# Optimization experiments

Measured on AMD Instinct MI355X. Metric: run time of the kernel, lower is better.

Reference implementation:

```python
import jax, jax.numpy as jnp
import numpy as np

B, S, D = 4, 4096, 1024

def setup_inputs() -> dict:
    key = jax.random.key(0)
    kx, kq, kk, kv = jax.random.split(key, 4)
    x = jax.random.normal(kx, (B, S, D), dtype=jnp.float32)
    # nn.Linear weights, stored here as [d_in, d_out] so y = x @ W
    scale = 1.0 / np.sqrt(D)
    Wq = jax.random.normal(kq, (D, D), dtype=jnp.float32) * scale
    Wk = jax.random.normal(kk, (D, D), dtype=jnp.float32) * scale
    Wv = jax.random.normal(kv, (D, D), dtype=jnp.float32) * scale
    return {"x": x, "Wq": Wq, "Wk": Wk, "Wv": Wv}

def reference(x, Wq, Wk, Wv):
    b, n, d_in = x.shape
    d_out = Wk.shape[1]
    q = jnp.einsum('bnd,de->bne', x, Wq)
    k = jnp.einsum('bnd,de,->bne', x, Wk, 1.0)  # keys
    v = jnp.einsum('bnd,de->bne', x, Wv)
    # full causal attention: scores scaled by 1/sqrt(d_out) AFTER masking (matches source)
    scores = jnp.einsum('bqe,bke->bqk', q, k)
    causal = jnp.triu(jnp.ones((n, n), dtype=bool), k=1)  # True above diagonal -> masked
    scores = jnp.where(causal[None, :, :], -jnp.inf, scores)
    attn = jax.nn.softmax(scores / jnp.sqrt(jnp.asarray(d_out, scores.dtype)), axis=-1)
    # dropout p=0.0 (eval) -> identity
    return jnp.einsum('bqk,bke->bqe', attn, v)
```

## Files before the change

### kernel.cpp

```cpp
#include <hip/hip_runtime.h>
#include <hip/hip_bf16.h>

#define B_ 4
#define S_ 4096
#define D_ 1024
#define NT_ 32
#define PAIRS_ 528

typedef __attribute__((ext_vector_type(8))) short short8;
typedef __attribute__((ext_vector_type(4))) float f32x4;

__device__ __forceinline__ unsigned short f2bf(float f) {
    union { float f; unsigned u; } v; v.f = f;
    unsigned u = v.u;
    return (unsigned short)((u + 0x7fffu + ((u >> 16) & 1u)) >> 16);
}

__device__ __forceinline__ void gld_lds16(const unsigned short* g, unsigned short* l) {
    __builtin_amdgcn_global_load_lds((const __attribute__((address_space(1))) void*)g,
                                     (__attribute__((address_space(3))) void*)l, 16, 0, 0);
}

__device__ __forceinline__ void stage128x32(const unsigned short* gbase, size_t ld,
                                            unsigned short* ls, int tid) {
    const int r = tid >> 2;
    const int c = (tid & 3) * 8;
    unsigned short* lw = ls + tid * 8;
    gld_lds16(gbase + (size_t)r * ld + c, lw);
    gld_lds16(gbase + (size_t)(r + 64) * ld + c, lw + 2048);
}

__global__ __launch_bounds__(256) void prep_x(const float* __restrict__ x,
                                              unsigned short* __restrict__ xb) {
    size_t i = ((size_t)blockIdx.x * 256 + threadIdx.x) * 8;
    float4 a = *(const float4*)&x[i];
    float4 b = *(const float4*)&x[i + 4];
    unsigned u0 = (unsigned)f2bf(a.x) | ((unsigned)f2bf(a.y) << 16);
    unsigned u1 = (unsigned)f2bf(a.z) | ((unsigned)f2bf(a.w) << 16);
    unsigned u2 = (unsigned)f2bf(b.x) | ((unsigned)f2bf(b.y) << 16);
    unsigned u3 = (unsigned)f2bf(b.z) | ((unsigned)f2bf(b.w) << 16);
    uint4 val; val.x = u0; val.y = u1; val.z = u2; val.w = u3;
    *(uint4*)&xb[i] = val;
}

__global__ __launch_bounds__(256) void prep_w(const float* __restrict__ Wq,
                                              const float* __restrict__ Wk,
                                              const float* __restrict__ Wv,
                                              unsigned short* __restrict__ Wt) {
    __shared__ float ls[64 * 65];
    const int z = blockIdx.z;
    const float* __restrict__ W = (z == 0) ? Wq : (z == 1) ? Wk : Wv;
    unsigned short* __restrict__ Wtz = Wt + (size_t)z * D_ * D_;
    const int k0 = blockIdx.y * 64, n0 = blockIdx.x * 64;
    const int tid = threadIdx.x;
    #pragma unroll
    for (int i = 0; i < 16; ++i) {
        int lin = i * 256 + tid, r = lin >> 6, c = lin & 63;
        ls[r * 65 + c] = W[(size_t)(k0 + r) * D_ + n0 + c];
    }
    __syncthreads();
    #pragma unroll
    for (int i = 0; i < 16; ++i) {
        int lin = i * 256 + tid, r = lin >> 6, c = lin & 63;
        Wtz[(size_t)(n0 + r) * D_ + k0 + c] = f2bf(ls[c * 65 + r]);
    }
}

__global__ __launch_bounds__(256) void qkv_gemm(
    const unsigned short* __restrict__ xb, const unsigned short* __restrict__ Wt,
    unsigned short* __restrict__ Q, unsigned short* __restrict__ K,
    unsigned short* __restrict__ V)
{
    __shared__ __align__(16) unsigned short lsA[4096];
    __shared__ __align__(16) unsigned short lsB[4096];

    const int z = blockIdx.z;
    unsigned short* __restrict__ Y = (z == 0) ? Q : (z == 1) ? K : V;
    const float scale = (z == 0) ? 0.03125f : 1.0f;

    const int m0 = blockIdx.y * 128, n0 = blockIdx.x * 128;
    const int tid = threadIdx.x, lane = tid & 63, w = tid >> 6;
    const int wm = w >> 1, wn = w & 1, quad = lane >> 4, ln = lane & 15;

    const unsigned short* Ab = xb + (size_t)m0 * D_;
    const unsigned short* Bb = Wt + (size_t)z * D_ * D_ + (size_t)n0 * D_;

    f32x4 acc[4][4] = {};

    for (int et = 0; et < D_ / 32; ++et) {
        stage128x32(Ab + et * 32, D_, lsA, tid);
        stage128x32(Bb + et * 32, D_, lsB, tid);
        __syncthreads();
        short8 af[4], bfr[4];
        #pragma unroll
        for (int mf = 0; mf < 4; ++mf)
            af[mf] = *(const short8*)&lsA[(wm * 64 + mf * 16 + ln) * 32 + quad * 8];
        #pragma unroll
        for (int nf = 0; nf < 4; ++nf)
            bfr[nf] = *(const short8*)&lsB[(wn * 64 + nf * 16 + ln) * 32 + quad * 8];
        #pragma unroll
        for (int mf = 0; mf < 4; ++mf)
            #pragma unroll
            for (int nf = 0; nf < 4; ++nf)
                acc[mf][nf] = __builtin_amdgcn_mfma_f32_16x16x32_bf16(af[mf], bfr[nf], acc[mf][nf], 0, 0, 0);
        __syncthreads();
    }

    #pragma unroll
    for (int mf = 0; mf < 4; ++mf)
        #pragma unroll
        for (int nf = 0; nf < 4; ++nf)
            #pragma unroll
            for (int r = 0; r < 4; ++r) {
                int row = m0 + wm * 64 + mf * 16 + quad * 4 + r;
                int col = n0 + wn * 64 + nf * 16 + ln;
                Y[(size_t)row * D_ + col] = f2bf(acc[mf][nf][r] * scale);
            }
}

__global__ __launch_bounds__(256) void vt_trans(const unsigned short* __restrict__ V,
                                                unsigned short* __restrict__ Vt) {
    __shared__ unsigned short ls[64 * 66];
    const int s0 = blockIdx.x * 64, e0 = blockIdx.y * 64, b = blockIdx.z;
    const int tid = threadIdx.x;
    const size_t base = (size_t)b * S_ * D_;
    #pragma unroll
    for (int i = 0; i < 16; ++i) {
        int lin = i * 256 + tid, r = lin >> 6, c = lin & 63;
        ls[r * 66 + c] = V[base + (size_t)(s0 + r) * D_ + e0 + c];
    }
    __syncthreads();
    const size_t baseT = (size_t)b * D_ * S_;
    #pragma unroll
    for (int i = 0; i < 16; ++i) {
        int lin = i * 256 + tid, r = lin >> 6, c = lin & 63;
        Vt[baseT + (size_t)(e0 + r) * S_ + s0 + c] = ls[c * 66 + r];
    }
}

__global__ __launch_bounds__(256) void qk_pexp(
    const unsigned short* __restrict__ Q, const unsigned short* __restrict__ K,
    unsigned short* __restrict__ P, float* __restrict__ lpart)
{
    __shared__ __align__(16) unsigned short lsA[4096];
    __shared__ __align__(16) unsigned short lsB[4096];
    __shared__ float sml[2][128];

    const int p = blockIdx.x, b = blockIdx.y;
    int qt = (int)((sqrtf(8.0f * (float)p + 1.0f) - 1.0f) * 0.5f);
    while ((qt + 1) * (qt + 2) / 2 <= p) ++qt;
    while (qt * (qt + 1) / 2 > p) --qt;
    const int kt = p - qt * (qt + 1) / 2;

    const int q0 = qt * 128, k0 = kt * 128;
    const int tid = threadIdx.x, lane = tid & 63, w = tid >> 6;
    const int wm = w >> 1, wn = w & 1, quad = lane >> 4, ln = lane & 15;
    const size_t base = (size_t)b * S_ * D_;

    const unsigned short* Qb = Q + base + (size_t)q0 * D_;
    const unsigned short* Kb = K + base + (size_t)k0 * D_;

    f32x4 acc[4][4] = {};
    for (int et = 0; et < D_ / 32; ++et) {
        stage128x32(Qb + et * 32, D_, lsA, tid);
        stage128x32(Kb + et * 32, D_, lsB, tid);
        __syncthreads();
        short8 af[4], bfr[4];
        #pragma unroll
        for (int mf = 0; mf < 4; ++mf)
            af[mf] = *(const short8*)&lsA[(wm * 64 + mf * 16 + ln) * 32 + quad * 8];
        #pragma unroll
        for (int nf = 0; nf < 4; ++nf)
            bfr[nf] = *(const short8*)&lsB[(wn * 64 + nf * 16 + ln) * 32 + quad * 8];
        #pragma unroll
        for (int mf = 0; mf < 4; ++mf)
            #pragma unroll
            for (int nf = 0; nf < 4; ++nf)
                acc[mf][nf] = __builtin_amdgcn_mfma_f32_16x16x32_bf16(af[mf], bfr[nf], acc[mf][nf], 0, 0, 0);
        __syncthreads();
    }

    const bool diag = (kt == qt);
    unsigned short* Pt = P + ((size_t)b * PAIRS_ + p) * (128 * 128);

    #pragma unroll
    for (int mf = 0; mf < 4; ++mf)
        #pragma unroll
        for (int r = 0; r < 4; ++r) {
            int rowq = wm * 64 + mf * 16 + quad * 4 + r;
            float lsum = 0.0f;
            #pragma unroll
            for (int nf = 0; nf < 4; ++nf) {
                int ckey = wn * 64 + nf * 16 + ln;
                float s = acc[mf][nf][r];
                float pe = (diag && ckey > rowq) ? 0.0f : __expf(fminf(s, 60.0f));
                Pt[rowq * 128 + ckey] = f2bf(pe);
                lsum += pe;
            }
            #pragma unroll
            for (int off = 1; off < 16; off <<= 1)
                lsum += __shfl_xor(lsum, off);
            if (ln == 0) sml[wn][rowq] = lsum;
        }
    __syncthreads();

    if (tid < 128)
        lpart[((size_t)b * PAIRS_ + p) * 128 + tid] = sml[0][tid] + sml[1][tid];
}

__global__ __launch_bounds__(128) void merge_il(const float* __restrict__ lpart,
                                                float* __restrict__ il) {
    const int qt = blockIdx.x, b = blockIdx.y;
    const int row = threadIdx.x;
    const int pbase = qt * (qt + 1) / 2;
    float l = 0.0f;
    for (int kt = 0; kt <= qt; ++kt)
        l += lpart[((size_t)b * PAIRS_ + pbase + kt) * 128 + row];
    il[(size_t)b * S_ + qt * 128 + row] = 1.0f / l;
}

__global__ __launch_bounds__(256) void pv_gemm(
    const unsigned short* __restrict__ P, const unsigned short* __restrict__ Vt,
    const float* __restrict__ il, float* __restrict__ O)
{
    __shared__ __align__(16) unsigned short lsA[4096];
    __shared__ __align__(16) unsigned short lsB[4096];

    const int dt = blockIdx.x, b = blockIdx.z;
    const int qt = NT_ - 1 - blockIdx.y;
    const int q0 = qt * 128, d0 = dt * 128;
    const int tid = threadIdx.x, lane = tid & 63, w = tid >> 6;
    const int wm = w >> 1, wn = w & 1, quad = lane >> 4, ln = lane & 15;
    const int pbase = qt * (qt + 1) / 2;

    const unsigned short* Vtb = Vt + ((size_t)b * D_ + d0) * S_;

    f32x4 acc[4][4] = {};

    for (int ktile = 0; ktile <= qt; ++ktile) {
        const unsigned short* Ptile = P + ((size_t)b * PAIRS_ + pbase + ktile) * (128 * 128);
        #pragma unroll 1
        for (int sub = 0; sub < 4; ++sub) {
            stage128x32(Ptile + sub * 32, 128, lsA, tid);
            stage128x32(Vtb + ktile * 128 + sub * 32, S_, lsB, tid);
            __syncthreads();
            short8 af[4], bfr[4];
            #pragma unroll
            for (int mf = 0; mf < 4; ++mf)
                af[mf] = *(const short8*)&lsA[(wm * 64 + mf * 16 + ln) * 32 + quad * 8];
            #pragma unroll
            for (int nf = 0; nf < 4; ++nf)
                bfr[nf] = *(const short8*)&lsB[(wn * 64 + nf * 16 + ln) * 32 + quad * 8];
            #pragma unroll
            for (int mf = 0; mf < 4; ++mf)
                #pragma unroll
                for (int nf = 0; nf < 4; ++nf)
                    acc[mf][nf] = __builtin_amdgcn_mfma_f32_16x16x32_bf16(af[mf], bfr[nf], acc[mf][nf], 0, 0, 0);
            __syncthreads();
        }
    }

    #pragma unroll
    for (int mf = 0; mf < 4; ++mf) {
        float ilv[4];
        #pragma unroll
        for (int r = 0; r < 4; ++r)
            ilv[r] = il[(size_t)b * S_ + q0 + wm * 64 + mf * 16 + quad * 4 + r];
        #pragma unroll
        for (int nf = 0; nf < 4; ++nf)
            #pragma unroll
            for (int r = 0; r < 4; ++r) {
                int rowq = q0 + wm * 64 + mf * 16 + quad * 4 + r;
                int col = d0 + wn * 64 + nf * 16 + ln;
                O[((size_t)b * S_ + rowq) * D_ + col] = acc[mf][nf][r] * ilv[r];
            }
    }
}

extern "C" void kernel_launch(void* const* d_in, const int* in_sizes, int n_in,
                              void* d_out, int out_size, void* d_ws, size_t ws_size,
                              hipStream_t stream) {
    const float* x  = (const float*)d_in[0];
    const float* Wq = (const float*)d_in[1];
    const float* Wk = (const float*)d_in[2];
    const float* Wv = (const float*)d_in[3];

    const size_t nQ = (size_t)B_ * S_ * D_;
    const size_t nP = (size_t)B_ * PAIRS_ * 128 * 128;

    unsigned short* P  = (unsigned short*)d_ws;
    unsigned short* V  = P;
    unsigned short* Q  = P + nP;
    unsigned short* K  = Q + nQ;
    unsigned short* Vt = K + nQ;
    unsigned short* xb = Vt;
    unsigned short* Wt = Vt + nQ;
    float* lpart = (float*)(Wt + (size_t)3 * D_ * D_);
    float* il    = lpart + (size_t)B_ * PAIRS_ * 128;
    float* O = (float*)d_out;

    hipLaunchKernelGGL(prep_x, dim3(8192), dim3(256), 0, stream, x, xb);
    hipLaunchKernelGGL(prep_w, dim3(16, 16, 3), dim3(256), 0, stream, Wq, Wk, Wv, Wt);
    hipLaunchKernelGGL(qkv_gemm, dim3(8, 128, 3), dim3(256), 0, stream, xb, Wt, Q, K, V);
    hipLaunchKernelGGL(vt_trans, dim3(64, 16, B_), dim3(256), 0, stream, V, Vt);
    hipLaunchKernelGGL(qk_pexp, dim3(PAIRS_, B_), dim3(256), 0, stream, Q, K, P, lpart);
    hipLaunchKernelGGL(merge_il, dim3(NT_, B_), dim3(128), 0, stream, lpart, il);
    hipLaunchKernelGGL(pv_gemm, dim3(8, NT_, B_), dim3(256), 0, stream, P, Vt, il, O);
}
```

Before: 496.3 us.

## Remap block indices for XCD locality and widen PV tiles to 128x256

Remaps block indices in qkv_gemm and qk_pexp so that blocks landing on the same XCD share operand tiles and the triangular (qt,kt) work is balanced across XCDs. pv_gemm now computes 128x256 output tiles with 32 accumulators per thread. Each staged P tile is reused across twice as many columns, and the grid shrinks to 512 blocks with a load-balanced qt assignment. This halves P re-reads from global memory, at the cost of more registers and LDS and possibly lower occupancy.

```diff
diff --git a/kernel.cpp b/kernel.cpp
--- a/kernel.cpp
+++ b/kernel.cpp
@@ -78,7 +78,12 @@
     unsigned short* __restrict__ Y = (z == 0) ? Q : (z == 1) ? K : V;
     const float scale = (z == 0) ? 0.03125f : 1.0f;
 
-    const int m0 = blockIdx.y * 128, n0 = blockIdx.x * 128;
+    const int lin = blockIdx.x + 8 * blockIdx.y;
+    const int xcd = lin & 7;
+    const int s = lin >> 3;
+    const int m0 = (xcd * 16 + (s >> 3)) * 128;
+    const int n0 = (s & 7) * 128;
+
     const int tid = threadIdx.x, lane = tid & 63, w = tid >> 6;
     const int wm = w >> 1, wn = w & 1, quad = lane >> 4, ln = lane & 15;
 
@@ -146,11 +151,15 @@
     __shared__ __align__(16) unsigned short lsB[4096];
     __shared__ float sml[2][128];
 
-    const int p = blockIdx.x, b = blockIdx.y;
-    int qt = (int)((sqrtf(8.0f * (float)p + 1.0f) - 1.0f) * 0.5f);
-    while ((qt + 1) * (qt + 2) / 2 <= p) ++qt;
-    while (qt * (qt + 1) / 2 > p) --qt;
-    const int kt = p - qt * (qt + 1) / 2;
+    const int l = blockIdx.x, b = blockIdx.y;
+    const int r = l & 7;
+    const int s = l >> 3;
+    int qt, kt;
+    if (s < r + 1)            { qt = r;      kt = s; }
+    else if (s < 33)          { qt = 31 - r; kt = s - (r + 1); }
+    else if (s < 42 + r)      { qt = 8 + r;  kt = s - 33; }
+    else                      { qt = 23 - r; kt = s - (42 + r); }
+    const int p = qt * (qt + 1) / 2 + kt;
 
     const int q0 = qt * 128, k0 = kt * 128;
     const int tid = threadIdx.x, lane = tid & 63, w = tid >> 6;
@@ -186,14 +195,14 @@
     #pragma unroll
     for (int mf = 0; mf < 4; ++mf)
         #pragma unroll
-        for (int r = 0; r < 4; ++r) {
-            int rowq = wm * 64 + mf * 16 + quad * 4 + r;
+        for (int rr = 0; rr < 4; ++rr) {
+            int rowq = wm * 64 + mf * 16 + quad * 4 + rr;
             float lsum = 0.0f;
             #pragma unroll
             for (int nf = 0; nf < 4; ++nf) {
                 int ckey = wn * 64 + nf * 16 + ln;
-                float s = acc[mf][nf][r];
-                float pe = (diag && ckey > rowq) ? 0.0f : __expf(fminf(s, 60.0f));
+                float sc = acc[mf][nf][rr];
+                float pe = (diag && ckey > rowq) ? 0.0f : __expf(fminf(sc, 60.0f));
                 Pt[rowq * 128 + ckey] = f2bf(pe);
                 lsum += pe;
             }
@@ -224,18 +233,25 @@
     const float* __restrict__ il, float* __restrict__ O)
 {
     __shared__ __align__(16) unsigned short lsA[4096];
-    __shared__ __align__(16) unsigned short lsB[4096];
-
-    const int dt = blockIdx.x, b = blockIdx.z;
-    const int qt = NT_ - 1 - blockIdx.y;
-    const int q0 = qt * 128, d0 = dt * 128;
+    __shared__ __align__(16) unsigned short lsB[8192];
+
+    const int l = blockIdx.x;
+    const int b = l >> 7;
+    const int l7 = l & 127;
+    const int r = l7 & 7;
+    const int s = l7 >> 3;
+    const int g = r >> 2;
+    const int dt = r & 3;
+    const int qt = (g == 0) ? ((s < 8) ? 31 - s : 15 - s) : (23 - s);
+
+    const int q0 = qt * 128, d0 = dt * 256;
     const int tid = threadIdx.x, lane = tid & 63, w = tid >> 6;
     const int wm = w >> 1, wn = w & 1, quad = lane >> 4, ln = lane & 15;
     const int pbase = qt * (qt + 1) / 2;
 
     const unsigned short* Vtb = Vt + ((size_t)b * D_ + d0) * S_;
 
-    f32x4 acc[4][4] = {};
+    f32x4 acc[4][8] = {};
 
     for (int ktile = 0; ktile <= qt; ++ktile) {
         const unsigned short* Ptile = P + ((size_t)b * PAIRS_ + pbase + ktile) * (128 * 128);
@@ -243,18 +259,19 @@
         for (int sub = 0; sub < 4; ++sub) {
             stage128x32(Ptile + sub * 32, 128, lsA, tid);
             stage128x32(Vtb + ktile * 128 + sub * 32, S_, lsB, tid);
+            stage128x32(Vtb + 128 * S_ + ktile * 128 + sub * 32, S_, lsB + 4096, tid);
             __syncthreads();
-            short8 af[4], bfr[4];
+            short8 af[4], bfr[8];
             #pragma unroll
             for (int mf = 0; mf < 4; ++mf)
                 af[mf] = *(const short8*)&lsA[(wm * 64 + mf * 16 + ln) * 32 + quad * 8];
             #pragma unroll
-            for (int nf = 0; nf < 4; ++nf)
-                bfr[nf] = *(const short8*)&lsB[(wn * 64 + nf * 16 + ln) * 32 + quad * 8];
+            for (int nf = 0; nf < 8; ++nf)
+                bfr[nf] = *(const short8*)&lsB[(wn * 128 + nf * 16 + ln) * 32 + quad * 8];
             #pragma unroll
             for (int mf = 0; mf < 4; ++mf)
                 #pragma unroll
-                for (int nf = 0; nf < 4; ++nf)
+                for (int nf = 0; nf < 8; ++nf)
                     acc[mf][nf] = __builtin_amdgcn_mfma_f32_16x16x32_bf16(af[mf], bfr[nf], acc[mf][nf], 0, 0, 0);
             __syncthreads();
         }
@@ -264,15 +281,15 @@
     for (int mf = 0; mf < 4; ++mf) {
         float ilv[4];
         #pragma unroll
-        for (int r = 0; r < 4; ++r)
-            ilv[r] = il[(size_t)b * S_ + q0 + wm * 64 + mf * 16 + quad * 4 + r];
-        #pragma unroll
-        for (int nf = 0; nf < 4; ++nf)
-            #pragma unroll
-            for (int r = 0; r < 4; ++r) {
-                int rowq = q0 + wm * 64 + mf * 16 + quad * 4 + r;
-                int col = d0 + wn * 64 + nf * 16 + ln;
-                O[((size_t)b * S_ + rowq) * D_ + col] = acc[mf][nf][r] * ilv[r];
+        for (int rr = 0; rr < 4; ++rr)
+            ilv[rr] = il[(size_t)b * S_ + q0 + wm * 64 + mf * 16 + quad * 4 + rr];
+        #pragma unroll
+        for (int nf = 0; nf < 8; ++nf)
+            #pragma unroll
+            for (int rr = 0; rr < 4; ++rr) {
+                int rowq = q0 + wm * 64 + mf * 16 + quad * 4 + rr;
+                int col = d0 + wn * 128 + nf * 16 + ln;
+                O[((size_t)b * S_ + rowq) * D_ + col] = acc[mf][nf][rr] * ilv[rr];
             }
     }
 }
@@ -305,5 +322,5 @@
     hipLaunchKernelGGL(vt_trans, dim3(64, 16, B_), dim3(256), 0, stream, V, Vt);
     hipLaunchKernelGGL(qk_pexp, dim3(PAIRS_, B_), dim3(256), 0, stream, Q, K, P, lpart);
     hipLaunchKernelGGL(merge_il, dim3(NT_, B_), dim3(128), 0, stream, lpart, il);
-    hipLaunchKernelGGL(pv_gemm, dim3(8, NT_, B_), dim3(256), 0, stream, P, Vt, il, O);
-}
+    hipLaunchKernelGGL(pv_gemm, dim3(512), dim3(256), 0, stream, P, Vt, il, O);
+}
```

Measured after the change: 533.5 us. 1.07x slower.
